# Kernel tuning notes

Hardware: AMD Instinct MI355X
Metric: run time of the kernel (lower is better)

Reference implementation:

```python
import jax, jax.numpy as jnp
import numpy as np

H = 16        # num query heads
HKV = 4       # num kv heads
D = 128       # head_dim
HID = 2048    # hidden_size
G = H // HKV  # heads per kv group


def setup_inputs() -> dict:
    key = jax.random.key(0)
    ks = jax.random.split(key, 9)
    s = 0.02
    x = jax.random.normal(ks[0], (2, 2048, HID), dtype=jnp.float32)
    wq = jax.random.normal(ks[1], (HID, H * D), dtype=jnp.float32) * s
    bq = jnp.zeros((H * D,), jnp.float32)
    wk = jax.random.normal(ks[2], (HID, HKV * D), dtype=jnp.float32) * s
    bk = jnp.zeros((HKV * D,), jnp.float32)
    wv = jax.random.normal(ks[3], (HID, HKV * D), dtype=jnp.float32) * s
    bv = jnp.zeros((HKV * D,), jnp.float32)
    wo = jax.random.normal(ks[4], (HID, HID), dtype=jnp.float32) * s
    bo = jnp.zeros((HID,), jnp.float32)
    return dict(x=x, wq=wq, bq=bq, wk=wk, bk=bk, wv=wv, bv=bv, wo=wo, bo=bo)


def reference(x, wq, bq, wk, bk, wv, bv, wo, bo):
    B, S, _ = x.shape
    scale = jnp.float32(1.0 / np.sqrt(D))
    # projections (torch Linear with weight stored as [in, out] here)
    q = (x @ wq + bq).reshape(B, S, H, D)          # [B,S,H,D]
    k = (x @ wk + bk).reshape(B, S, HKV, D)        # [B,S,Hkv,D]
    v = (x @ wv + bv).reshape(B, S, HKV, D)
    # group query heads by kv head instead of expanding KV
    q = q.reshape(B, S, HKV, G, D)
    scores = jnp.einsum('bqhgd,bkhd->bhgqk', q, k) * scale  # [B,Hkv,G,S,S]
    causal = jnp.triu(jnp.ones((S, S), dtype=bool), k=1)
    scores = jnp.where(causal, jnp.float32(-1e9), scores)
    weights = jax.nn.softmax(scores, axis=-1)
    out = jnp.einsum('bhgqk,bkhd->bqhgd', weights, v)        # [B,S,Hkv,G,D]
    out = out.reshape(B, S, H * D)
    return out @ wo + bo
```

## Files before the change

kernel.cpp:

```cpp
#include <hip/hip_runtime.h>
#include <hip/hip_bf16.h>
#include <math.h>

#define HID 2048
#define NH 16
#define NKV 4
#define HD 128
#define GQ 4
#define BATCH 2

typedef short short8v __attribute__((ext_vector_type(8)));
typedef float f32x4 __attribute__((ext_vector_type(4)));

__device__ __forceinline__ ushort f2bf(float f) {
  uint u = __float_as_uint(f);
  uint r = (u + 0x7fffu + ((u >> 16) & 1u)) >> 16;
  return (ushort)r;
}

__device__ __forceinline__ void gld_lds16(const void* g, void* lds) {
  __builtin_amdgcn_global_load_lds(
      (const __attribute__((address_space(1))) unsigned int*)g,
      (__attribute__((address_space(3))) unsigned int*)lds, 16, 0, 0);
}

#define WAVE_LDS_FENCE()                                \
  do {                                                  \
    asm volatile("s_waitcnt lgkmcnt(0)" ::: "memory");  \
    __builtin_amdgcn_sched_barrier(0);                  \
  } while (0)

__global__ __launch_bounds__(256) void castx_kernel(
    const float* __restrict__ x, ushort* __restrict__ xb) {
  const int i = ((int)blockIdx.x * 256 + (int)threadIdx.x) * 8;
  float4 f0 = *reinterpret_cast<const float4*>(x + i);
  float4 f1 = *reinterpret_cast<const float4*>(x + i + 4);
  uint4 o;
  o.x = (uint)f2bf(f0.x) | ((uint)f2bf(f0.y) << 16);
  o.y = (uint)f2bf(f0.z) | ((uint)f2bf(f0.w) << 16);
  o.z = (uint)f2bf(f1.x) | ((uint)f2bf(f1.y) << 16);
  o.w = (uint)f2bf(f1.z) | ((uint)f2bf(f1.w) << 16);
  *reinterpret_cast<uint4*>(xb + i) = o;
}

__global__ __launch_bounds__(256) void tcast_kernel(
    const float* __restrict__ W, ushort* __restrict__ Wt, int K, int N) {
  __shared__ float T[32][33];
  const int k0 = blockIdx.x * 32;
  const int n0 = blockIdx.y * 32;
  const int t = threadIdx.x;
  const int r = t >> 3;
  const int c4 = (t & 7) * 4;
  float4 vin = *reinterpret_cast<const float4*>(
      &W[(size_t)(k0 + r) * N + n0 + c4]);
  T[c4 + 0][r] = vin.x;
  T[c4 + 1][r] = vin.y;
  T[c4 + 2][r] = vin.z;
  T[c4 + 3][r] = vin.w;
  __syncthreads();
  ushort4 o;
  o.x = f2bf(T[r][c4 + 0]);
  o.y = f2bf(T[r][c4 + 1]);
  o.z = f2bf(T[r][c4 + 2]);
  o.w = f2bf(T[r][c4 + 3]);
  *reinterpret_cast<ushort4*>(&Wt[(size_t)(n0 + r) * K + k0 + c4]) = o;
}

template <int MODE>
__global__ __launch_bounds__(256) void gemm_big(
    const ushort* __restrict__ A,
    const ushort* __restrict__ W0, const ushort* __restrict__ W1,
    const ushort* __restrict__ W2,
    const float* __restrict__ b0, const float* __restrict__ b1,
    const float* __restrict__ b2,
    void* __restrict__ C0, void* __restrict__ C1, void* __restrict__ C2,
    int M, int K, int S) {
  __shared__ ushort As[2][128 * 32];
  __shared__ ushort Bs[2][128 * 32];
  const int tid = threadIdx.x;
  const int m0 = blockIdx.y * 128;
  const int n0 = blockIdx.x * 128;
  const int wave = tid >> 6;
  const int lane = tid & 63;
  const int quad = lane >> 4;
  const int lr = lane & 15;
  const int l4 = lane >> 2;
  const int lc = (lane & 3) * 8;
  const int wm = (wave >> 1) * 64;
  const int wn = (wave & 1) * 64;

  const ushort* Wt;
  const float* bias;
  int nloc, Nout, om;
  void* Cout;
  if (MODE == 0) {
    Wt = W0; bias = b0; nloc = n0; Nout = 2048; om = 0; Cout = C0;
  } else {
    if (n0 < 2048)      { Wt = W0; bias = b0; nloc = n0;        Nout = 2048; om = 1; Cout = C0; }
    else if (n0 < 2560) { Wt = W1; bias = b1; nloc = n0 - 2048; Nout = 512;  om = 1; Cout = C1; }
    else                { Wt = W2; bias = b2; nloc = n0 - 2560; Nout = 512;  om = 2; Cout = C2; }
  }

  f32x4 acc[4][4];
#pragma unroll
  for (int i = 0; i < 4; ++i)
#pragma unroll
    for (int j = 0; j < 4; ++j) acc[i][j] = (f32x4){0.f, 0.f, 0.f, 0.f};

  const size_t rowA = (size_t)(m0 + wave * 32 + l4) * K + lc;
  const size_t rowB = (size_t)(nloc + wave * 32 + l4) * K + lc;

#define STAGE_GEMM(t, bi)                                                  \
  do {                                                                     \
    const int kof = (t) * 32;                                              \
    gld_lds16(&A[rowA + kof], &As[bi][(wave * 32) * 32]);                  \
    gld_lds16(&A[rowA + 16 * K + kof], &As[bi][(wave * 32 + 16) * 32]);    \
    gld_lds16(&Wt[rowB + kof], &Bs[bi][(wave * 32) * 32]);                 \
    gld_lds16(&Wt[rowB + 16 * K + kof], &Bs[bi][(wave * 32 + 16) * 32]);   \
  } while (0)

  const int nt = K / 32;
  STAGE_GEMM(0, 0);

  for (int t = 0; t < nt; ++t) {
    const int cur = t & 1;
    __builtin_amdgcn_s_barrier();
    if (t + 1 < nt) {
      STAGE_GEMM(t + 1, cur ^ 1);
      asm volatile("s_waitcnt vmcnt(4)" ::: "memory");
    } else {
      asm volatile("s_waitcnt vmcnt(0)" ::: "memory");
    }
    __builtin_amdgcn_s_barrier();
    __builtin_amdgcn_sched_barrier(0);

    short8v af[4], bf[4];
#pragma unroll
    for (int x = 0; x < 4; ++x) {
      const int ra = wm + x * 16 + lr;
      af[x] = *reinterpret_cast<const short8v*>(&As[cur][ra * 32 + quad * 8]);
      const int rb = wn + x * 16 + lr;
      bf[x] = *reinterpret_cast<const short8v*>(&Bs[cur][rb * 32 + quad * 8]);
    }
#pragma unroll
    for (int i = 0; i < 4; ++i)
#pragma unroll
      for (int j = 0; j < 4; ++j)
        acc[i][j] = __builtin_amdgcn_mfma_f32_16x16x32_bf16(
            af[i], bf[j], acc[i][j], 0, 0, 0);
  }
#undef STAGE_GEMM

#pragma unroll
  for (int i = 0; i < 4; ++i) {
    const int row_base = m0 + wm + i * 16 + quad * 4;
#pragma unroll
    for (int j = 0; j < 4; ++j) {
      const int col = nloc + wn + j * 16 + lr;
      const float b = bias[col];
      if (om == 0) {
        float* C = (float*)Cout;
#pragma unroll
        for (int rg = 0; rg < 4; ++rg)
          C[(size_t)(row_base + rg) * Nout + col] = acc[i][j][rg] + b;
      } else if (om == 1) {
        ushort* C = (ushort*)Cout;
#pragma unroll
        for (int rg = 0; rg < 4; ++rg)
          C[(size_t)(row_base + rg) * Nout + col] = f2bf(acc[i][j][rg] + b);
      } else {
        ushort* C = (ushort*)Cout;
        const int bb = (row_base >= S) ? 1 : 0;
        const int s = row_base - bb * S;
        const int kvh = col >> 7;
        const int d = col & 127;
        ushort4 o;
        o.x = f2bf(acc[i][j][0] + b);
        o.y = f2bf(acc[i][j][1] + b);
        o.z = f2bf(acc[i][j][2] + b);
        o.w = f2bf(acc[i][j][3] + b);
        *reinterpret_cast<ushort4*>(
            &C[((size_t)(bb * NKV + kvh) * HD + d) * S + s]) = o;
      }
    }
  }
}

__device__ __forceinline__ void stage_kv_dma8(
    const ushort* __restrict__ Kb, const ushort* __restrict__ Vb,
    ushort* Kdst, ushort* Vdst, int k0, int S, int wave, int lane) {
  const int rK = lane >> 4, cK = lane & 15;
  const int rV = lane >> 3, cV = lane & 7;
#pragma unroll
  for (int c = 0; c < 2; ++c) {
    const int g = wave * 2 + c;
    const int row = g * 4 + rK;
    const int jk = cK ^ (row & 15);
    gld_lds16(&Kb[(size_t)(k0 + row) * (NKV * HD) + jk * 8], &Kdst[g * 512]);
    const int d = g * 8 + rV;
    const int jv = cV ^ (d & 7);
    gld_lds16(&Vb[(size_t)d * S + k0 + jv * 8], &Vdst[g * 512]);
  }
}

__global__ __launch_bounds__(512, 4) void gqa_attn_mfma(
    const ushort* __restrict__ Qg, const ushort* __restrict__ Kgl,
    const ushort* __restrict__ Vt_g, ushort* __restrict__ O, int S) {
  __shared__ __align__(16) ushort L[32768];
  ushort* K0 = L;
  ushort* K1 = L + 8192;
  ushort* V0 = L + 16384;
  ushort* V1 = L + 24576;

  const int tid = threadIdx.x;
  const int wave = tid >> 6;
  const int lane = tid & 63;
  const int quad = lane >> 4;
  const int lr = lane & 15;
  const int q0 = ((int)gridDim.x - 1 - (int)blockIdx.x) * 128;
  const int hq = blockIdx.y;
  const int b = blockIdx.z;
  const int kvh = hq >> 2;
  const float scale = 0.08838834764831845f;

  const ushort* Qb = Qg + ((size_t)b * S) * (NH * HD) + (size_t)hq * HD;
  const ushort* Kb = Kgl + ((size_t)b * S) * (NKV * HD) + (size_t)kvh * HD;
  const ushort* Vb = Vt_g + ((size_t)(b * NKV + kvh) * HD) * S;

#pragma unroll
  for (int i = 0; i < 4; ++i) {
    const int id = tid + i * 512;
    const int r = id >> 4, c = id & 15;
    const int p = c ^ (r & 15);
    *reinterpret_cast<uint4*>(&L[r * 128 + p * 8]) =
        *reinterpret_cast<const uint4*>(
            &Qb[(size_t)(q0 + r) * (NH * HD) + c * 8]);
  }
  __syncthreads();
  short8v aq[4];
  {
    const int ra = wave * 16 + lr;
#pragma unroll
    for (int ks = 0; ks < 4; ++ks)
      aq[ks] = *reinterpret_cast<const short8v*>(
          &L[ra * 128 + (((ks * 4 + quad) ^ lr) & 15) * 8]);
  }
  __syncthreads();

  f32x4 oacc[8];
#pragma unroll
  for (int nb = 0; nb < 8; ++nb) oacc[nb] = (f32x4){0.f, 0.f, 0.f, 0.f};
  float l_r = 0.f;

  const int ntiles = q0 / 64 + 2;

  const int laneA = ((quad * 2) & 3) * 16 + lr;
  const int laneB = ((quad * 2 + 1) & 3) * 16 + lr;
  const bool hi = (quad >= 2);

  stage_kv_dma8(Kb, Vb, K0, V0, 0, S, wave, lane);

  for (int kt = 0; kt < ntiles; ++kt) {
    const int k0 = kt * 64;
    const ushort* Kc = (kt & 1) ? K1 : K0;
    const ushort* Vc = (kt & 1) ? V1 : V0;

    __builtin_amdgcn_s_barrier();
    if (kt + 1 < ntiles) {
      ushort* Kn = (kt & 1) ? K0 : K1;
      ushort* Vn = (kt & 1) ? V0 : V1;
      stage_kv_dma8(Kb, Vb, Kn, Vn, k0 + 64, S, wave, lane);
      asm volatile("s_waitcnt vmcnt(4)" ::: "memory");
    } else {
      asm volatile("s_waitcnt vmcnt(0)" ::: "memory");
    }
    __builtin_amdgcn_s_barrier();
    __builtin_amdgcn_sched_barrier(0);

    f32x4 sacc[4];
    __builtin_amdgcn_s_setprio(1);
#pragma unroll
    for (int nb = 0; nb < 4; ++nb) {
      sacc[nb] = (f32x4){0.f, 0.f, 0.f, 0.f};
      const int rb = nb * 16 + lr;
#pragma unroll
      for (int ks = 0; ks < 4; ++ks) {
        short8v bk = *reinterpret_cast<const short8v*>(
            &Kc[rb * 128 + (((ks * 4 + quad) ^ lr) & 15) * 8]);
        sacc[nb] = __builtin_amdgcn_mfma_f32_16x16x32_bf16(
            bk, aq[ks], sacc[nb], 0, 0, 0);
      }
    }
    __builtin_amdgcn_s_setprio(0);

    const bool needmask = (kt + 2 >= ntiles);
    const int qi = q0 + wave * 16 + lr;
    uint u[4][2];
    float rs = 0.f;
#pragma unroll
    for (int nb = 0; nb < 4; ++nb) {
      float p[4];
#pragma unroll
      for (int rg = 0; rg < 4; ++rg) {
        float sv = sacc[nb][rg] * scale;
        if (needmask) {
          const int kj = k0 + nb * 16 + quad * 4 + rg;
          if (kj > qi) sv = -1e30f;
        }
        p[rg] = __expf(sv);
        rs += p[rg];
      }
      u[nb][0] = (uint)f2bf(p[0]) | ((uint)f2bf(p[1]) << 16);
      u[nb][1] = (uint)f2bf(p[2]) | ((uint)f2bf(p[3]) << 16);
    }
    rs += __shfl_xor(rs, 16);
    rs += __shfl_xor(rs, 32);
    l_r += rs;

    short8v ap[2];
#pragma unroll
    for (int ks = 0; ks < 2; ++ks) {
      const uint w0a = __shfl(u[2 * ks + 0][0], laneA);
      const uint w0b = __shfl(u[2 * ks + 1][0], laneA);
      const uint w1a = __shfl(u[2 * ks + 0][1], laneA);
      const uint w1b = __shfl(u[2 * ks + 1][1], laneA);
      const uint w2a = __shfl(u[2 * ks + 0][0], laneB);
      const uint w2b = __shfl(u[2 * ks + 1][0], laneB);
      const uint w3a = __shfl(u[2 * ks + 0][1], laneB);
      const uint w3b = __shfl(u[2 * ks + 1][1], laneB);
      uint4 q4;
      q4.x = hi ? w0b : w0a;
      q4.y = hi ? w1b : w1a;
      q4.z = hi ? w2b : w2a;
      q4.w = hi ? w3b : w3a;
      ap[ks] = *reinterpret_cast<short8v*>(&q4);
    }

    __builtin_amdgcn_s_setprio(1);
#pragma unroll
    for (int nb = 0; nb < 8; ++nb) {
      const int rv = nb * 16 + lr;
#pragma unroll
      for (int ks = 0; ks < 2; ++ks) {
        short8v bv = *reinterpret_cast<const short8v*>(
            &Vc[rv * 64 + (((ks * 4 + quad) ^ lr) & 7) * 8]);
        oacc[nb] = __builtin_amdgcn_mfma_f32_16x16x32_bf16(
            ap[ks], bv, oacc[nb], 0, 0, 0);
      }
    }
    __builtin_amdgcn_s_setprio(0);
  }

  const float invl = 1.0f / l_r;
  float inv[4];
#pragma unroll
  for (int rg = 0; rg < 4; ++rg)
    inv[rg] = __shfl(invl, (lane & 48) | (quad * 4 + rg));
  __syncthreads();
  ushort* ow = &L[wave * 16 * 128];
#pragma unroll
  for (int nb = 0; nb < 8; ++nb)
#pragma unroll
    for (int rg = 0; rg < 4; ++rg)
      ow[(quad * 4 + rg) * 128 + nb * 16 + lr] = f2bf(oacc[nb][rg] * inv[rg]);
  WAVE_LDS_FENCE();
  ushort* Ob = O + ((size_t)b * S) * (NH * HD) + (size_t)hq * HD;
#pragma unroll
  for (int ii = 0; ii < 4; ++ii) {
    const int id = lane + ii * 64;
    const int r16 = id >> 4, c = id & 15;
    uint4 val = *reinterpret_cast<const uint4*>(&ow[r16 * 128 + c * 8]);
    *reinterpret_cast<uint4*>(
        &Ob[(size_t)(q0 + wave * 16 + r16) * (NH * HD) + c * 8]) = val;
  }
}

extern "C" void kernel_launch(void* const* d_in, const int* in_sizes, int n_in,
                              void* d_out, int out_size, void* d_ws,
                              size_t ws_size, hipStream_t stream) {
  const float* x = (const float*)d_in[0];
  const float* wq = (const float*)d_in[1];
  const float* bq = (const float*)d_in[2];
  const float* wk = (const float*)d_in[3];
  const float* bk = (const float*)d_in[4];
  const float* wv = (const float*)d_in[5];
  const float* bv = (const float*)d_in[6];
  const float* wo = (const float*)d_in[7];
  const float* bo = (const float*)d_in[8];
  float* out = (float*)d_out;

  const int M = in_sizes[0] / HID;
  const int S = M / BATCH;

  char* w = (char*)d_ws;
  ushort* xb    = (ushort*)(w + 0);
  ushort* qb    = (ushort*)(w + (16u << 20));
  ushort* kb    = (ushort*)(w + (32u << 20));
  ushort* vT    = (ushort*)(w + (36u << 20));
  ushort* attnb = (ushort*)(w + (40u << 20));
  ushort* wqT   = (ushort*)(w + (56u << 20));
  ushort* wkT   = (ushort*)(w + (64u << 20));
  ushort* wvT   = (ushort*)(w + (66u << 20));
  ushort* woT   = (ushort*)(w + (68u << 20));

  dim3 blk(256);
  castx_kernel<<<dim3((M * HID) / (8 * 256)), blk, 0, stream>>>(x, xb);
  tcast_kernel<<<dim3(HID / 32, (NH * HD) / 32), blk, 0, stream>>>(
      wq, wqT, HID, NH * HD);
  tcast_kernel<<<dim3(HID / 32, (NKV * HD) / 32), blk, 0, stream>>>(
      wk, wkT, HID, NKV * HD);
  tcast_kernel<<<dim3(HID / 32, (NKV * HD) / 32), blk, 0, stream>>>(
      wv, wvT, HID, NKV * HD);
  tcast_kernel<<<dim3(HID / 32, HID / 32), blk, 0, stream>>>(
      wo, woT, HID, HID);

  gemm_big<1><<<dim3(3072 / 128, M / 128), blk, 0, stream>>>(
      xb, wqT, wkT, wvT, bq, bk, bv, qb, kb, vT, M, HID, S);

  gqa_attn_mfma<<<dim3(S / 128, NH, BATCH), dim3(512), 0, stream>>>(
      qb, kb, vT, attnb, S);

  gemm_big<0><<<dim3(HID / 128, M / 128), blk, 0, stream>>>(
      attnb, woT, nullptr, nullptr, bo, nullptr, nullptr,
      out, nullptr, nullptr, M, HID, S);
}
```

Measured before the change: 333.9 us.

## Split long causal query tiles across two KV ranges with atomic merge

```diff
diff --git a/kernel.cpp b/kernel.cpp
--- a/kernel.cpp
+++ b/kernel.cpp
@@ -29,6 +29,11 @@
     asm volatile("s_waitcnt lgkmcnt(0)" ::: "memory");  \
     __builtin_amdgcn_sched_barrier(0);                  \
   } while (0)
+
+__device__ const int QT_TAB[24] = {7, 8, 9, 10, 11, 12, 13, 14, 15, 15, 6, 14,
+                                   5, 13, 4, 12, 3, 11, 2, 10, 1, 9, 0, 8};
+__device__ const int LO_TAB[24] = {0, 0, 0, 0, 0, 0, 0, 0, 0, 16, 0, 16,
+                                   0, 16, 0, 16, 0, 16, 0, 16, 0, 16, 0, 16};
 
 __global__ __launch_bounds__(256) void castx_kernel(
     const float* __restrict__ x, ushort* __restrict__ xb) {
@@ -64,6 +69,32 @@
   o.z = f2bf(T[r][c4 + 2]);
   o.w = f2bf(T[r][c4 + 3]);
   *reinterpret_cast<ushort4*>(&Wt[(size_t)(n0 + r) * K + k0 + c4]) = o;
+}
+
+__global__ __launch_bounds__(256) void zero_kernel(float4* __restrict__ p) {
+  p[(size_t)blockIdx.x * 256 + threadIdx.x] = (float4){0.f, 0.f, 0.f, 0.f};
+}
+
+__global__ __launch_bounds__(256) void merge_kernel(
+    const float* __restrict__ Oacc, const float* __restrict__ Lacc,
+    ushort* __restrict__ attnb) {
+  const int i = (int)blockIdx.x * 256 + (int)threadIdx.x;
+  const int d8 = i & 15;
+  const int h = (i >> 4) & 15;
+  const int r = i >> 8;
+  const float invl = 1.0f / Lacc[r * NH + h];
+  const float* src = Oacc + ((size_t)r * (NH * HD)) + h * HD + d8 * 8;
+  float4 a0 = *reinterpret_cast<const float4*>(src);
+  float4 a1 = *reinterpret_cast<const float4*>(src + 4);
+  uint4 o;
+  o.x = (uint)f2bf(a0.x * invl) | ((uint)f2bf(a0.y * invl) << 16);
+  o.y = (uint)f2bf(a0.z * invl) | ((uint)f2bf(a0.w * invl) << 16);
+  o.z = (uint)f2bf(a1.x * invl) | ((uint)f2bf(a1.y * invl) << 16);
+  o.w = (uint)f2bf(a1.z * invl) | ((uint)f2bf(a1.w * invl) << 16);
+  const int b = r >> 10;
+  const int s = 1024 + (r & 1023);
+  *reinterpret_cast<uint4*>(
+      &attnb[((size_t)(b * 2048 + s)) * (NH * HD) + h * HD + d8 * 8]) = o;
 }
 
 template <int MODE>
@@ -205,7 +236,8 @@
 
 __global__ __launch_bounds__(512, 4) void gqa_attn_mfma(
     const ushort* __restrict__ Qg, const ushort* __restrict__ Kgl,
-    const ushort* __restrict__ Vt_g, ushort* __restrict__ O, int S) {
+    const ushort* __restrict__ Vt_g, ushort* __restrict__ O,
+    float* __restrict__ Oacc, float* __restrict__ Lacc, int S) {
   __shared__ __align__(16) ushort L[32768];
   ushort* K0 = L;
   ushort* K1 = L + 8192;
@@ -217,9 +249,15 @@
   const int lane = tid & 63;
   const int quad = lane >> 4;
   const int lr = lane & 15;
-  const int q0 = ((int)gridDim.x - 1 - (int)blockIdx.x) * 128;
-  const int hq = blockIdx.y;
-  const int b = blockIdx.z;
+  const int item = blockIdx.z;
+  const int qt = QT_TAB[item];
+  const int lo = LO_TAB[item];
+  const int ntf = 2 * qt + 2;
+  const int hi = lo ? ntf : (ntf < 16 ? ntf : 16);
+  const bool part = (qt >= 8);
+  const int q0 = qt * 128;
+  const int hq = blockIdx.x;
+  const int b = blockIdx.y;
   const int kvh = hq >> 2;
   const float scale = 0.08838834764831845f;
 
@@ -252,21 +290,20 @@
   for (int nb = 0; nb < 8; ++nb) oacc[nb] = (f32x4){0.f, 0.f, 0.f, 0.f};
   float l_r = 0.f;
 
-  const int ntiles = q0 / 64 + 2;
-
   const int laneA = ((quad * 2) & 3) * 16 + lr;
   const int laneB = ((quad * 2 + 1) & 3) * 16 + lr;
-  const bool hi = (quad >= 2);
-
-  stage_kv_dma8(Kb, Vb, K0, V0, 0, S, wave, lane);
-
-  for (int kt = 0; kt < ntiles; ++kt) {
+  const bool hihalf = (quad >= 2);
+
+  stage_kv_dma8(Kb, Vb, (lo & 1) ? K1 : K0, (lo & 1) ? V1 : V0, lo * 64, S,
+                wave, lane);
+
+  for (int kt = lo; kt < hi; ++kt) {
     const int k0 = kt * 64;
     const ushort* Kc = (kt & 1) ? K1 : K0;
     const ushort* Vc = (kt & 1) ? V1 : V0;
 
     __builtin_amdgcn_s_barrier();
-    if (kt + 1 < ntiles) {
+    if (kt + 1 < hi) {
       ushort* Kn = (kt & 1) ? K0 : K1;
       ushort* Vn = (kt & 1) ? V0 : V1;
       stage_kv_dma8(Kb, Vb, Kn, Vn, k0 + 64, S, wave, lane);
@@ -293,7 +330,7 @@
     }
     __builtin_amdgcn_s_setprio(0);
 
-    const bool needmask = (kt + 2 >= ntiles);
+    const bool needmask = (kt >= 2 * qt);
     const int qi = q0 + wave * 16 + lr;
     uint u[4][2];
     float rs = 0.f;
@@ -329,10 +366,10 @@
       const uint w3a = __shfl(u[2 * ks + 0][1], laneB);
       const uint w3b = __shfl(u[2 * ks + 1][1], laneB);
       uint4 q4;
-      q4.x = hi ? w0b : w0a;
-      q4.y = hi ? w1b : w1a;
-      q4.z = hi ? w2b : w2a;
-      q4.w = hi ? w3b : w3a;
+      q4.x = hihalf ? w0b : w0a;
+      q4.y = hihalf ? w1b : w1a;
+      q4.z = hihalf ? w2b : w2a;
+      q4.w = hihalf ? w3b : w3a;
       ap[ks] = *reinterpret_cast<short8v*>(&q4);
     }
 
@@ -351,27 +388,44 @@
     __builtin_amdgcn_s_setprio(0);
   }
 
-  const float invl = 1.0f / l_r;
-  float inv[4];
-#pragma unroll
-  for (int rg = 0; rg < 4; ++rg)
-    inv[rg] = __shfl(invl, (lane & 48) | (quad * 4 + rg));
-  __syncthreads();
-  ushort* ow = &L[wave * 16 * 128];
-#pragma unroll
-  for (int nb = 0; nb < 8; ++nb)
+  if (part) {
+    float* Oa = Oacc +
+                ((size_t)(b * 1024 + (q0 - 1024) + wave * 16 + quad * 4)) *
+                    (NH * HD) +
+                hq * HD;
+#pragma unroll
+    for (int nb = 0; nb < 8; ++nb)
+#pragma unroll
+      for (int rg = 0; rg < 4; ++rg)
+        atomicAdd(&Oa[(size_t)rg * (NH * HD) + nb * 16 + lr], oacc[nb][rg]);
+    if (quad == 0)
+      atomicAdd(
+          &Lacc[(size_t)(b * 1024 + (q0 - 1024) + wave * 16 + lr) * NH + hq],
+          l_r);
+  } else {
+    const float invl = 1.0f / l_r;
+    float inv[4];
 #pragma unroll
     for (int rg = 0; rg < 4; ++rg)
-      ow[(quad * 4 + rg) * 128 + nb * 16 + lr] = f2bf(oacc[nb][rg] * inv[rg]);
-  WAVE_LDS_FENCE();
-  ushort* Ob = O + ((size_t)b * S) * (NH * HD) + (size_t)hq * HD;
-#pragma unroll
-  for (int ii = 0; ii < 4; ++ii) {
-    const int id = lane + ii * 64;
-    const int r16 = id >> 4, c = id & 15;
-    uint4 val = *reinterpret_cast<const uint4*>(&ow[r16 * 128 + c * 8]);
-    *reinterpret_cast<uint4*>(
-        &Ob[(size_t)(q0 + wave * 16 + r16) * (NH * HD) + c * 8]) = val;
+      inv[rg] = __shfl(invl, (lane & 48) | (quad * 4 + rg));
+    __syncthreads();
+    ushort* ow = &L[wave * 16 * 128];
+#pragma unroll
+    for (int nb = 0; nb < 8; ++nb)
+#pragma unroll
+      for (int rg = 0; rg < 4; ++rg)
+        ow[(quad * 4 + rg) * 128 + nb * 16 + lr] =
+            f2bf(oacc[nb][rg] * inv[rg]);
+    WAVE_LDS_FENCE();
+    ushort* Ob = O + ((size_t)b * S) * (NH * HD) + (size_t)hq * HD;
+#pragma unroll
+    for (int ii = 0; ii < 4; ++ii) {
+      const int id = lane + ii * 64;
+      const int r16 = id >> 4, c = id & 15;
+      uint4 val = *reinterpret_cast<const uint4*>(&ow[r16 * 128 + c * 8]);
+      *reinterpret_cast<uint4*>(
+          &Ob[(size_t)(q0 + wave * 16 + r16) * (NH * HD) + c * 8]) = val;
+    }
   }
 }
 
@@ -402,6 +456,8 @@
   ushort* wkT   = (ushort*)(w + (64u << 20));
   ushort* wvT   = (ushort*)(w + (66u << 20));
   ushort* woT   = (ushort*)(w + (68u << 20));
+  float* Oacc = (float*)(w + 0);
+  float* Lacc = (float*)(w + (64u << 20));
 
   dim3 blk(256);
   castx_kernel<<<dim3((M * HID) / (8 * 256)), blk, 0, stream>>>(x, xb);
@@ -417,8 +473,13 @@
   gemm_big<1><<<dim3(3072 / 128, M / 128), blk, 0, stream>>>(
       xb, wqT, wkT, wvT, bq, bk, bv, qb, kb, vT, M, HID, S);
 
-  gqa_attn_mfma<<<dim3(S / 128, NH, BATCH), dim3(512), 0, stream>>>(
-      qb, kb, vT, attnb, S);
+  zero_kernel<<<dim3(4096), blk, 0, stream>>>((float4*)Oacc);
+  zero_kernel<<<dim3(32), blk, 0, stream>>>((float4*)Lacc);
+
+  gqa_attn_mfma<<<dim3(NH, BATCH, 24), dim3(512), 0, stream>>>(
+      qb, kb, vT, attnb, Oacc, Lacc, S);
+
+  merge_kernel<<<dim3(2048), blk, 0, stream>>>(Oacc, Lacc, attnb);
 
   gemm_big<0><<<dim3(HID / 128, M / 128), blk, 0, stream>>>(
       attnb, woT, nullptr, nullptr, bo, nullptr, nullptr,
```

New measurement: 330.9 us. Within noise of the previous version (-0.9%).
